# Kernel optimization log

Measured on AMD Instinct MI355X. Metric: run time of the kernel, lower is better.

Reference implementation:

```python
import jax, jax.numpy as jnp
import numpy as np

# static config (matches init_kwargs and spatial_shapes input)
SPATIAL = ((100, 100), (50, 50), (25, 25), (13, 13))  # (H, W) per level
D_MODEL, N_HEADS, N_LEVELS, N_POINTS, D_FFN = 256, 8, 4, 4, 1024
D_HEAD = D_MODEL // N_HEADS
LEN_IN = sum(h * w for h, w in SPATIAL)
LEVEL_START = np.cumsum([0] + [h * w for h, w in SPATIAL])[:-1]


def setup_inputs() -> dict:
    key = jax.random.key(0)
    ks = jax.random.split(key, 12)
    N = 2
    f = lambda k, shape, s=0.02: jax.random.normal(k, shape, jnp.float32) * s
    return {
        "src": jax.random.normal(ks[0], (N, LEN_IN, D_MODEL), jnp.float32),
        "pos": jax.random.normal(ks[1], (N, LEN_IN, D_MODEL), jnp.float32),
        "reference_points": jax.random.uniform(ks[2], (N, LEN_IN, N_LEVELS, 2), jnp.float32),
        "spatial_shapes": jnp.asarray(SPATIAL, jnp.int32),
        "level_start_index": jnp.asarray(LEVEL_START, jnp.int32),
        "W_value": f(ks[3], (D_MODEL, D_MODEL)),
        "b_value": jnp.zeros((D_MODEL,), jnp.float32),
        "W_off": f(ks[4], (D_MODEL, N_HEADS * N_LEVELS * N_POINTS * 2)),
        "b_off": f(ks[5], (N_HEADS * N_LEVELS * N_POINTS * 2,), 0.5),
        "W_attn": f(ks[6], (D_MODEL, N_HEADS * N_LEVELS * N_POINTS)),
        "b_attn": jnp.zeros((N_HEADS * N_LEVELS * N_POINTS,), jnp.float32),
        "W_out": f(ks[7], (D_MODEL, D_MODEL)),
        "b_out": jnp.zeros((D_MODEL,), jnp.float32),
        "W1": f(ks[8], (D_MODEL, D_FFN)),
        "b1": jnp.zeros((D_FFN,), jnp.float32),
        "W2": f(ks[9], (D_FFN, D_MODEL)),
        "b2": jnp.zeros((D_MODEL,), jnp.float32),
        "g1": jnp.ones((D_MODEL,), jnp.float32),
        "be1": jnp.zeros((D_MODEL,), jnp.float32),
        "g2": jnp.ones((D_MODEL,), jnp.float32),
        "be2": jnp.zeros((D_MODEL,), jnp.float32),
    }


def _ln(x, g, b, eps=1e-5):
    mu = x.mean(-1, keepdims=True)
    var = ((x - mu) ** 2).mean(-1, keepdims=True)
    return (x - mu) * jax.lax.rsqrt(var + eps) * g + b


def _bilinear(v, loc, H, W):
    # v: [N, heads, H*W, Dh]; loc: [N, Lq, heads, P, 2] normalized to [0,1]
    # replicates F.grid_sample(align_corners=False, padding_mode='zeros') with grid=2*loc-1
    N, Lq, Hh, P, _ = loc.shape
    x = loc[..., 0] * W - 0.5
    y = loc[..., 1] * H - 0.5
    x0 = jnp.floor(x)
    y0 = jnp.floor(y)
    wx1 = x - x0
    wy1 = y - y0
    x0i = x0.astype(jnp.int32)
    y0i = y0.astype(jnp.int32)
    out = jnp.zeros((N, Lq, Hh, P, v.shape[-1]), v.dtype)
    for dy, dx in ((0, 0), (0, 1), (1, 0), (1, 1)):
        xi = x0i + dx
        yi = y0i + dy
        w = (wx1 if dx else 1.0 - wx1) * (wy1 if dy else 1.0 - wy1)
        valid = (xi >= 0) & (xi < W) & (yi >= 0) & (yi < H)
        idx = jnp.clip(yi, 0, H - 1) * W + jnp.clip(xi, 0, W - 1)  # [N,Lq,Hh,P]
        idx = idx.transpose(0, 2, 1, 3).reshape(N, Hh, Lq * P)
        g = jax.vmap(jax.vmap(lambda vm, im: vm[im]))(v, idx)  # [N,Hh,Lq*P,Dh]
        g = g.reshape(N, Hh, Lq, P, -1).transpose(0, 2, 1, 3, 4)
        out = out + (w * valid)[..., None] * g
    return out


def reference(src, pos, reference_points, spatial_shapes, level_start_index,
              W_value, b_value, W_off, b_off, W_attn, b_attn, W_out, b_out,
              W1, b1, W2, b2, g1, be1, g2, be2):
    N, Lq, _ = src.shape
    value = (src @ W_value + b_value).reshape(N, Lq, N_HEADS, D_HEAD)
    q = src + pos  # with_pos_embed
    off = (q @ W_off + b_off).reshape(N, Lq, N_HEADS, N_LEVELS, N_POINTS, 2)
    attn = (q @ W_attn + b_attn).reshape(N, Lq, N_HEADS, N_LEVELS * N_POINTS)
    attn = jax.nn.softmax(attn, axis=-1).reshape(N, Lq, N_HEADS, N_LEVELS, N_POINTS)
    # offset_normalizer = (W, H) per level
    normalizer = jnp.asarray([[w, h] for h, w in SPATIAL], jnp.float32)
    loc = reference_points[:, :, None, :, None, :] + off / normalizer[None, None, None, :, None, :]
    out = jnp.zeros((N, Lq, N_HEADS, D_HEAD), jnp.float32)
    for l, (H, W) in enumerate(SPATIAL):
        s = int(LEVEL_START[l])
        v_l = value[:, s:s + H * W].transpose(0, 2, 1, 3)  # [N, heads, H*W, Dh]
        samp = _bilinear(v_l, loc[:, :, :, l], H, W)       # [N, Lq, heads, P, Dh]
        out = out + jnp.einsum('nqhp,nqhpc->nqhc', attn[:, :, :, l], samp)
    src2 = out.reshape(N, Lq, D_MODEL) @ W_out + b_out
    x = _ln(src + src2, g1, be1)
    ffn = jax.nn.relu(x @ W1 + b1) @ W2 + b2
    return _ln(x + ffn, g2, be2)
```

## Files before the change

kernel.cpp:

```cpp
#include <hip/hip_runtime.h>
#include <hip/hip_bf16.h>
#include <cstdint>

#define D_MODEL   256
#define N_HEADS   8
#define N_LEVELS  4
#define N_POINTS  4
#define D_FFN     1024
#define D_HEAD    32
#define LEN_IN    13294
#define NBATCH    2
#define M_TOK     (NBATCH * LEN_IN)
#define M_PAD     26624

__constant__ int c_lvl_h[4] = {100, 50, 25, 13};
__constant__ int c_lvl_w[4] = {100, 50, 25, 13};
__constant__ int c_lvl_s[4] = {0, 10000, 12500, 13125};

typedef __attribute__((ext_vector_type(8))) __bf16 bf16x8;
typedef __attribute__((ext_vector_type(4))) __bf16 bf16x4;
typedef __attribute__((ext_vector_type(2))) __bf16 bf16x2;
typedef __attribute__((ext_vector_type(4))) float  f32x4;
typedef __attribute__((ext_vector_type(4))) uint32_t u32x4;

__device__ __forceinline__ float bflo(uint32_t w) { return __uint_as_float(w << 16); }
__device__ __forceinline__ float bfhi(uint32_t w) { return __uint_as_float(w & 0xffff0000u); }

__device__ __forceinline__ void lds_direct16(const void* g, void* l) {
    __builtin_amdgcn_global_load_lds(
        (const __attribute__((address_space(1))) uint32_t*)(uintptr_t)g,
        (__attribute__((address_space(3))) uint32_t*)(uintptr_t)l,
        16, 0, 0);
}

__global__ __launch_bounds__(256) void cvt_src_q(
    const float4* __restrict__ src, const float4* __restrict__ pos,
    bf16x4* __restrict__ sb, bf16x4* __restrict__ qb, int n4)
{
    const int i = blockIdx.x * 256 + threadIdx.x;
    if (i >= n4) return;
    const float4 s = src[i];
    const float4 p = pos[i];
    bf16x4 sv = { (__bf16)s.x, (__bf16)s.y, (__bf16)s.z, (__bf16)s.w };
    bf16x4 qv = { (__bf16)(s.x + p.x), (__bf16)(s.y + p.y),
                  (__bf16)(s.z + p.z), (__bf16)(s.w + p.w) };
    sb[i] = sv;
    qb[i] = qv;
}

__global__ __launch_bounds__(256) void transpose_all(
    const float* __restrict__ s0, const float* __restrict__ s1, const float* __restrict__ s2,
    const float* __restrict__ s3, const float* __restrict__ s4, const float* __restrict__ s5,
    __bf16* __restrict__ d0, __bf16* __restrict__ d1, __bf16* __restrict__ d2,
    __bf16* __restrict__ d3, __bf16* __restrict__ d4, __bf16* __restrict__ d5,
    const float* __restrict__ b_off, const float* __restrict__ b_attn,
    float* __restrict__ bias_oa)
{
    const int tx = threadIdx.x;
    const int ty = threadIdx.y;
    const int tid = ty * 32 + tx;
    const int b = blockIdx.x;
    if (b == 736) {
        if (tid < 256) bias_oa[tid] = b_off[tid];
        if (tid < 128) bias_oa[256 + tid] = b_attn[tid];
        return;
    }
    const int starts[7] = {0, 64, 128, 160, 224, 480, 736};
    const int Ks[6] = {256, 256, 256, 256, 256, 1024};
    const int Ns[6] = {256, 256, 128, 256, 1024, 256};
    const float* srcs[6] = {s0, s1, s2, s3, s4, s5};
    __bf16* dsts[6] = {d0, d1, d2, d3, d4, d5};
    int i = 0;
    while (b >= starts[i + 1]) ++i;
    const int t = b - starts[i];
    const int K = Ks[i], N = Ns[i];
    const float* W = srcs[i];
    __bf16* Wt = dsts[i];
    const int ntx = N >> 5;
    const int n0 = (t % ntx) * 32;
    const int k0 = (t / ntx) * 32;

    __shared__ float tl[32][33];
    #pragma unroll
    for (int j = 0; j < 4; ++j)
        tl[ty + j * 8][tx] = W[(size_t)(k0 + ty + j * 8) * N + n0 + tx];
    __syncthreads();
    #pragma unroll
    for (int j = 0; j < 4; ++j)
        Wt[(size_t)(n0 + ty + j * 8) * K + k0 + tx] = (__bf16)tl[tx][ty + j * 8];
}

template <typename OutT, bool RELU, int NP, int K>
__global__ __launch_bounds__(256) void gemm_mfma(
    const __bf16* __restrict__ A, const __bf16* __restrict__ Bt,
    const float* __restrict__ bias, OutT* __restrict__ C,
    int M, int N)
{
    __shared__ __bf16 As[NP * 128 * 32];
    __shared__ __bf16 Bs[NP * 128 * 32];

    const int tid  = threadIdx.x;
    const int lane = tid & 63;
    const int wv   = tid >> 6;
    const int bm   = blockIdx.y * 128;
    const int bn   = blockIdx.x * 128;
    const int wm   = (wv >> 1) * 64;
    const int wn   = (wv & 1) * 64;
    const int srow = lane >> 2;
    const int skc  = (lane & 3) * 8;
    const int fm   = lane & 15;
    const int fko  = (lane >> 4) * 8;

    f32x4 acc[4][4] = {};

    #pragma unroll
    for (int k0 = 0; k0 < K; k0 += 32 * NP) {
        #pragma unroll
        for (int p = 0; p < NP; ++p) {
            #pragma unroll
            for (int c = 0; c < 2; ++c) {
                const int r = wv * 32 + c * 16;
                lds_direct16(A  + (size_t)(bm + r + srow) * K + k0 + p * 32 + skc, As + p * 4096 + r * 32);
                lds_direct16(Bt + (size_t)(bn + r + srow) * K + k0 + p * 32 + skc, Bs + p * 4096 + r * 32);
            }
        }
        __syncthreads();

        #pragma unroll
        for (int p = 0; p < NP; ++p) {
            bf16x8 af[4], bfr[4];
            #pragma unroll
            for (int t = 0; t < 4; ++t) {
                af[t]  = *(const bf16x8*)(As + p * 4096 + (wm + t * 16 + fm) * 32 + fko);
                bfr[t] = *(const bf16x8*)(Bs + p * 4096 + (wn + t * 16 + fm) * 32 + fko);
            }
            #pragma unroll
            for (int mt = 0; mt < 4; ++mt)
                #pragma unroll
                for (int nt = 0; nt < 4; ++nt)
                    acc[mt][nt] = __builtin_amdgcn_mfma_f32_16x16x32_bf16(
                        af[mt], bfr[nt], acc[mt][nt], 0, 0, 0);
        }
        __syncthreads();
    }

    const int ecol = lane & 15;
    const int erow = (lane >> 4) * 4;
    #pragma unroll
    for (int nt = 0; nt < 4; ++nt) {
        const int col = bn + wn + nt * 16 + ecol;
        const float bv = bias[col];
        #pragma unroll
        for (int mt = 0; mt < 4; ++mt) {
            #pragma unroll
            for (int r = 0; r < 4; ++r) {
                const int row = bm + wm + mt * 16 + erow + r;
                if (row < M) {
                    float v = acc[mt][nt][r] + bv;
                    if (RELU) v = fmaxf(v, 0.f);
                    C[(size_t)row * N + col] = (OutT)v;
                }
            }
        }
    }
}

struct alignas(8) IW { uint32_t idx; float wt; };

__global__ __launch_bounds__(256) void msda_sample(
    const __bf16* __restrict__ value,
    const __bf16* __restrict__ oa,
    const float* __restrict__ refp,
    __bf16* __restrict__ out)
{
    __shared__ IW    sc[8][16][4];
    __shared__ float sw[8][16];

    const int row = blockIdx.x;
    const int tid = threadIdx.x;

    uint32_t cidx[4];
    float    cwt[4];
    const int h  = tid >> 4;
    const int lp = tid & 15;

    if (tid < 128) {
        const int l  = lp >> 2;
        const int Ww = c_lvl_w[l];
        const int Hh = c_lvl_h[l];
        const uint32_t opk = *(const uint32_t*)(oa + (size_t)row * 384 + h * 32 + lp * 2);
        const float ox = bflo(opk), oy = bfhi(opk);
        const float rx = refp[((size_t)row * 4 + l) * 2 + 0];
        const float ry = refp[((size_t)row * 4 + l) * 2 + 1];
        const float x = (rx + ox / (float)Ww) * (float)Ww - 0.5f;
        const float y = (ry + oy / (float)Hh) * (float)Hh - 0.5f;
        const float xf = floorf(x), yf = floorf(y);
        const float fx = x - xf,    fy = y - yf;
        const int x0 = (int)xf, y0 = (int)yf;
        const int n  = row / LEN_IN;
        const int base = n * LEN_IN + c_lvl_s[l];
        #pragma unroll
        for (int c = 0; c < 4; ++c) {
            const int dx = c & 1, dy = c >> 1;
            const int xi = x0 + dx, yi = y0 + dy;
            const bool valid = (xi >= 0) & (xi < Ww) & (yi >= 0) & (yi < Hh);
            cidx[c] = valid ? (uint32_t)(base + yi * Ww + xi) * 256u : 0u;
            cwt[c]  = valid ? (dx ? fx : 1.f - fx) * (dy ? fy : 1.f - fy) : 0.f;
        }
    } else if (tid < 136) {
        const int h2 = tid - 128;
        const __bf16* ap = oa + (size_t)row * 384 + 256 + h2 * 16;
        float e[16], mx = -1e30f;
        #pragma unroll
        for (int i = 0; i < 16; ++i) { e[i] = (float)ap[i]; mx = fmaxf(mx, e[i]); }
        float s = 0.f;
        #pragma unroll
        for (int i = 0; i < 16; ++i) { e[i] = __expf(e[i] - mx); s += e[i]; }
        const float inv = 1.f / s;
        #pragma unroll
        for (int i = 0; i < 16; ++i) sw[h2][i] = e[i] * inv;
    }
    __syncthreads();
    if (tid < 128) {
        const float a = sw[h][lp];
        IW w0 = { cidx[0], cwt[0] * a };
        IW w1 = { cidx[1], cwt[1] * a };
        IW w2 = { cidx[2], cwt[2] * a };
        IW w3 = { cidx[3], cwt[3] * a };
        u32x4 pk0 = { w0.idx, __float_as_uint(w0.wt), w1.idx, __float_as_uint(w1.wt) };
        u32x4 pk1 = { w2.idx, __float_as_uint(w2.wt), w3.idx, __float_as_uint(w3.wt) };
        *(u32x4*)&sc[h][lp][0] = pk0;
        *(u32x4*)&sc[h][lp][2] = pk1;
    }
    __syncthreads();

    const uint16_t* __restrict__ vu = (const uint16_t*)value;
    const int gh  = tid >> 5;
    const uint32_t col = (uint32_t)tid;
    float acc = 0.f;
    #pragma unroll
    for (int q = 0; q < 16; ++q) {
        const u32x4 a = *(const u32x4*)&sc[gh][q][0];
        const u32x4 b = *(const u32x4*)&sc[gh][q][2];
        acc += __uint_as_float(a.y) * __uint_as_float((uint32_t)vu[a.x + col] << 16);
        acc += __uint_as_float(a.w) * __uint_as_float((uint32_t)vu[a.z + col] << 16);
        acc += __uint_as_float(b.y) * __uint_as_float((uint32_t)vu[b.x + col] << 16);
        acc += __uint_as_float(b.w) * __uint_as_float((uint32_t)vu[b.z + col] << 16);
    }
    out[(size_t)row * 256 + tid] = (__bf16)acc;
}

template <bool BF16OUT, bool BBF16>
__global__ __launch_bounds__(256) void add_ln(
    const float4* __restrict__ a, const void* __restrict__ braw,
    const float4* __restrict__ g4, const float4* __restrict__ be4,
    float4* __restrict__ out, bf16x4* __restrict__ outb)
{
    const int tid  = threadIdx.x;
    const int row  = blockIdx.x * 4 + (tid >> 6);
    const int lane = tid & 63;
    const size_t e = (size_t)row * 64 + lane;
    const float4 va = a[e];
    float4 vb;
    if (BBF16) {
        const bf16x4 t = ((const bf16x4*)braw)[e];
        vb = { (float)t[0], (float)t[1], (float)t[2], (float)t[3] };
    } else {
        vb = ((const float4*)braw)[e];
    }
    float4 v = { va.x + vb.x, va.y + vb.y, va.z + vb.z, va.w + vb.w };

    float s  = v.x + v.y + v.z + v.w;
    float s2 = v.x * v.x + v.y * v.y + v.z * v.z + v.w * v.w;
    #pragma unroll
    for (int o = 32; o > 0; o >>= 1) {
        s  += __shfl_down(s, o);
        s2 += __shfl_down(s2, o);
    }
    s  = __shfl(s, 0);
    s2 = __shfl(s2, 0);
    const float mu  = s * (1.f / 256.f);
    const float var = s2 * (1.f / 256.f) - mu * mu;
    const float rs  = rsqrtf(var + 1e-5f);
    const float4 g = g4[lane];
    const float4 be = be4[lane];
    float4 o;
    o.x = (v.x - mu) * rs * g.x + be.x;
    o.y = (v.y - mu) * rs * g.y + be.y;
    o.z = (v.z - mu) * rs * g.z + be.z;
    o.w = (v.w - mu) * rs * g.w + be.w;
    out[e] = o;
    if (BF16OUT) {
        bf16x4 ob = { (__bf16)o.x, (__bf16)o.y, (__bf16)o.z, (__bf16)o.w };
        outb[e] = ob;
    }
}

extern "C" void kernel_launch(void* const* d_in, const int* in_sizes, int n_in,
                              void* d_out, int out_size, void* d_ws, size_t ws_size,
                              hipStream_t stream)
{
    const float* src     = (const float*)d_in[0];
    const float* pos     = (const float*)d_in[1];
    const float* refp    = (const float*)d_in[2];
    const float* W_value = (const float*)d_in[5];
    const float* b_value = (const float*)d_in[6];
    const float* W_off   = (const float*)d_in[7];
    const float* b_off   = (const float*)d_in[8];
    const float* W_attn  = (const float*)d_in[9];
    const float* b_attn  = (const float*)d_in[10];
    const float* W_out   = (const float*)d_in[11];
    const float* b_out   = (const float*)d_in[12];
    const float* W1      = (const float*)d_in[13];
    const float* b1      = (const float*)d_in[14];
    const float* W2      = (const float*)d_in[15];
    const float* b2      = (const float*)d_in[16];
    const float* g1      = (const float*)d_in[17];
    const float* be1     = (const float*)d_in[18];
    const float* g2      = (const float*)d_in[19];
    const float* be2     = (const float*)d_in[20];
    float* outp = (float*)d_out;

    const int M = M_TOK;
    char* ws = (char*)d_ws;
    const size_t R2 = (size_t)M_PAD * 512;

    __bf16* src_b = (__bf16*)(ws);
    __bf16* q_b   = (__bf16*)(ws + R2);
    __bf16* val_b = (__bf16*)(ws + 2 * R2);
    __bf16* oa    = (__bf16*)(ws + 3 * R2);
    __bf16* samp  = (__bf16*)(ws + 9 * R2 / 2);
    __bf16* src2b = (__bf16*)(ws + 11 * R2 / 2);
    __bf16* f2b   = (__bf16*)(ws + 11 * R2 / 2);
    float*  x     = (float*)(ws + 13 * R2 / 2);
    __bf16* x_b   = (__bf16*)(ws + 17 * R2 / 2);
    __bf16* hbuf  = (__bf16*)(ws);
    __bf16* wbase = (__bf16*)(ws + 19 * R2 / 2);
    __bf16* Wt_value = wbase;
    __bf16* Wt_oa    = wbase + 65536;
    __bf16* Wt_out   = wbase + 163840;
    __bf16* Wt1      = wbase + 229376;
    __bf16* Wt2      = wbase + 491520;
    float*  bias_oa  = (float*)(wbase + 753664);

    const dim3 blk(256);
    const int n4 = M * 256 / 4;

    cvt_src_q<<<dim3((n4 + 255) / 256), blk, 0, stream>>>(
        (const float4*)src, (const float4*)pos, (bf16x4*)src_b, (bf16x4*)q_b, n4);
    transpose_all<<<dim3(737), dim3(32, 8), 0, stream>>>(
        W_value, W_off, W_attn, W_out, W1, W2,
        Wt_value, Wt_oa, Wt_oa + 65536, Wt_out, Wt1, Wt2,
        b_off, b_attn, bias_oa);

    const int gm = M_PAD / 128;

    gemm_mfma<__bf16, false, 2, 256><<<dim3(2, gm), blk, 0, stream>>>(src_b, Wt_value, b_value, val_b, M, 256);
    gemm_mfma<__bf16, false, 2, 256><<<dim3(3, gm), blk, 0, stream>>>(q_b,   Wt_oa,    bias_oa, oa,    M, 384);

    msda_sample<<<dim3(M), blk, 0, stream>>>(val_b, oa, refp, samp);

    gemm_mfma<__bf16, false, 2, 256><<<dim3(2, gm), blk, 0, stream>>>(samp, Wt_out, b_out, src2b, M, 256);
    add_ln<true, true><<<dim3(M / 4), blk, 0, stream>>>(
        (const float4*)src, (const void*)src2b, (const float4*)g1, (const float4*)be1,
        (float4*)x, (bf16x4*)x_b);
    gemm_mfma<__bf16, true,  2, 256><<<dim3(8, gm), blk, 0, stream>>>(x_b,  Wt1, b1, hbuf, M, 1024);
    gemm_mfma<__bf16, false, 2, 1024><<<dim3(2, gm), blk, 0, stream>>>(hbuf, Wt2, b2, f2b, M, 256);
    add_ln<false, true><<<dim3(M / 4), blk, 0, stream>>>(
        (const float4*)x, (const void*)f2b, (const float4*)g2, (const float4*)be2,
        (float4*)outp, nullptr);
}
```

Baseline: 349.5 us.

## Fuse layernorms into output GEMMs and merge prep and front GEMM launches

Merges the weight-transpose and src/pos conversion kernels into one launch, and runs the value and offset/attention projections as one GEMM grid. Adds a gemm_ln kernel that computes a full 256-column row tile, then adds bias and residual and applies LayerNorm in the epilogue. This replaces the separate add_ln passes and drops the fp32 intermediate x buffer. The residuals are now read from bf16 copies (src_b, x_b) instead of fp32, which costs some accuracy. The sampler switches to byte-offset indexing and unrolling is dropped on the GEMM K loop.

```diff
diff --git a/kernel.cpp b/kernel.cpp
--- a/kernel.cpp
+++ b/kernel.cpp
@@ -19,7 +19,6 @@
 
 typedef __attribute__((ext_vector_type(8))) __bf16 bf16x8;
 typedef __attribute__((ext_vector_type(4))) __bf16 bf16x4;
-typedef __attribute__((ext_vector_type(2))) __bf16 bf16x2;
 typedef __attribute__((ext_vector_type(4))) float  f32x4;
 typedef __attribute__((ext_vector_type(4))) uint32_t u32x4;
 
@@ -33,38 +32,37 @@
         16, 0, 0);
 }
 
-__global__ __launch_bounds__(256) void cvt_src_q(
-    const float4* __restrict__ src, const float4* __restrict__ pos,
-    bf16x4* __restrict__ sb, bf16x4* __restrict__ qb, int n4)
-{
-    const int i = blockIdx.x * 256 + threadIdx.x;
-    if (i >= n4) return;
-    const float4 s = src[i];
-    const float4 p = pos[i];
-    bf16x4 sv = { (__bf16)s.x, (__bf16)s.y, (__bf16)s.z, (__bf16)s.w };
-    bf16x4 qv = { (__bf16)(s.x + p.x), (__bf16)(s.y + p.y),
-                  (__bf16)(s.z + p.z), (__bf16)(s.w + p.w) };
-    sb[i] = sv;
-    qb[i] = qv;
-}
-
-__global__ __launch_bounds__(256) void transpose_all(
+__global__ __launch_bounds__(256) void prep(
     const float* __restrict__ s0, const float* __restrict__ s1, const float* __restrict__ s2,
     const float* __restrict__ s3, const float* __restrict__ s4, const float* __restrict__ s5,
     __bf16* __restrict__ d0, __bf16* __restrict__ d1, __bf16* __restrict__ d2,
     __bf16* __restrict__ d3, __bf16* __restrict__ d4, __bf16* __restrict__ d5,
     const float* __restrict__ b_off, const float* __restrict__ b_attn,
-    float* __restrict__ bias_oa)
-{
-    const int tx = threadIdx.x;
-    const int ty = threadIdx.y;
-    const int tid = ty * 32 + tx;
+    float* __restrict__ bias_oa,
+    const float4* __restrict__ src, const float4* __restrict__ pos,
+    bf16x4* __restrict__ sb, bf16x4* __restrict__ qb, int n4)
+{
+    const int tid = threadIdx.x;
     const int b = blockIdx.x;
+    if (b >= 737) {
+        const int i = (b - 737) * 256 + tid;
+        if (i >= n4) return;
+        const float4 s = src[i];
+        const float4 p = pos[i];
+        bf16x4 sv = { (__bf16)s.x, (__bf16)s.y, (__bf16)s.z, (__bf16)s.w };
+        bf16x4 qv = { (__bf16)(s.x + p.x), (__bf16)(s.y + p.y),
+                      (__bf16)(s.z + p.z), (__bf16)(s.w + p.w) };
+        sb[i] = sv;
+        qb[i] = qv;
+        return;
+    }
     if (b == 736) {
         if (tid < 256) bias_oa[tid] = b_off[tid];
         if (tid < 128) bias_oa[256 + tid] = b_attn[tid];
         return;
     }
+    const int tx = tid & 31;
+    const int ty = tid >> 5;
     const int starts[7] = {0, 64, 128, 160, 224, 480, 736};
     const int Ks[6] = {256, 256, 256, 256, 256, 1024};
     const int Ns[6] = {256, 256, 128, 256, 1024, 256};
@@ -91,10 +89,10 @@
 }
 
 template <typename OutT, bool RELU, int NP, int K>
-__global__ __launch_bounds__(256) void gemm_mfma(
+__device__ __forceinline__ void gemm_core(
     const __bf16* __restrict__ A, const __bf16* __restrict__ Bt,
     const float* __restrict__ bias, OutT* __restrict__ C,
-    int M, int N)
+    int M, int N, int bm, int bn)
 {
     __shared__ __bf16 As[NP * 128 * 32];
     __shared__ __bf16 Bs[NP * 128 * 32];
@@ -102,8 +100,6 @@
     const int tid  = threadIdx.x;
     const int lane = tid & 63;
     const int wv   = tid >> 6;
-    const int bm   = blockIdx.y * 128;
-    const int bn   = blockIdx.x * 128;
     const int wm   = (wv >> 1) * 64;
     const int wn   = (wv & 1) * 64;
     const int srow = lane >> 2;
@@ -113,7 +109,6 @@
 
     f32x4 acc[4][4] = {};
 
-    #pragma unroll
     for (int k0 = 0; k0 < K; k0 += 32 * NP) {
         #pragma unroll
         for (int p = 0; p < NP; ++p) {
@@ -165,7 +160,155 @@
     }
 }
 
-struct alignas(8) IW { uint32_t idx; float wt; };
+template <typename OutT, bool RELU, int NP, int K>
+__global__ __launch_bounds__(256) void gemm_mfma(
+    const __bf16* __restrict__ A, const __bf16* __restrict__ Bt,
+    const float* __restrict__ bias, OutT* __restrict__ C, int M, int N)
+{
+    gemm_core<OutT, RELU, NP, K>(A, Bt, bias, C, M, N, blockIdx.y * 128, blockIdx.x * 128);
+}
+
+__global__ __launch_bounds__(256) void gemm_front(
+    const __bf16* __restrict__ A0, const __bf16* __restrict__ B0,
+    const float* __restrict__ bi0, __bf16* __restrict__ C0,
+    const __bf16* __restrict__ A1, const __bf16* __restrict__ B1,
+    const float* __restrict__ bi1, __bf16* __restrict__ C1, int M)
+{
+    const int bx = blockIdx.x;
+    if (bx < 2)
+        gemm_core<__bf16, false, 2, 256>(A0, B0, bi0, C0, M, 256, blockIdx.y * 128, bx * 128);
+    else
+        gemm_core<__bf16, false, 2, 256>(A1, B1, bi1, C1, M, 384, blockIdx.y * 128, (bx - 2) * 128);
+}
+
+template <typename OutT, int K>
+__global__ __launch_bounds__(256) void gemm_ln(
+    const __bf16* __restrict__ A, const __bf16* __restrict__ Bt,
+    const float* __restrict__ bias, const __bf16* __restrict__ res,
+    const float* __restrict__ gamma, const float* __restrict__ beta,
+    OutT* __restrict__ Cout, int M)
+{
+    constexpr int NP = 2;
+    __shared__ __bf16 As[NP * 64 * 32];
+    __shared__ __bf16 Bs[NP * 256 * 32];
+    __shared__ float lnsum[64][4];
+    __shared__ float lnsq[64][4];
+    __shared__ float lnstat[64][2];
+
+    const int tid  = threadIdx.x;
+    const int lane = tid & 63;
+    const int wv   = tid >> 6;
+    const int bm   = blockIdx.x * 64;
+    const int wn   = wv * 64;
+    const int srow = lane >> 2;
+    const int skc  = (lane & 3) * 8;
+    const int fm   = lane & 15;
+    const int fko  = (lane >> 4) * 8;
+
+    f32x4 acc[4][4] = {};
+
+    for (int k0 = 0; k0 < K; k0 += 32 * NP) {
+        #pragma unroll
+        for (int p = 0; p < NP; ++p) {
+            if (wv == 0) {  }
+            lds_direct16(A + (size_t)(bm + wv * 16 + srow) * K + k0 + p * 32 + skc,
+                         As + p * 2048 + (wv * 16) * 32);
+            #pragma unroll
+            for (int c = 0; c < 4; ++c) {
+                const int r = wv * 64 + c * 16;
+                lds_direct16(Bt + (size_t)(r + srow) * K + k0 + p * 32 + skc,
+                             Bs + p * 8192 + r * 32);
+            }
+        }
+        __syncthreads();
+
+        #pragma unroll
+        for (int p = 0; p < NP; ++p) {
+            bf16x8 af[4], bfr[4];
+            #pragma unroll
+            for (int t = 0; t < 4; ++t) {
+                af[t]  = *(const bf16x8*)(As + p * 2048 + (t * 16 + fm) * 32 + fko);
+                bfr[t] = *(const bf16x8*)(Bs + p * 8192 + (wn + t * 16 + fm) * 32 + fko);
+            }
+            #pragma unroll
+            for (int mt = 0; mt < 4; ++mt)
+                #pragma unroll
+                for (int nt = 0; nt < 4; ++nt)
+                    acc[mt][nt] = __builtin_amdgcn_mfma_f32_16x16x32_bf16(
+                        af[mt], bfr[nt], acc[mt][nt], 0, 0, 0);
+        }
+        __syncthreads();
+    }
+
+    const int ecol = lane & 15;
+    const int erow = (lane >> 4) * 4;
+
+    float g4[4], b4[4];
+    #pragma unroll
+    for (int nt = 0; nt < 4; ++nt) {
+        const int col = wn + nt * 16 + ecol;
+        g4[nt] = gamma[col];
+        b4[nt] = beta[col];
+        const float bv = bias[col];
+        #pragma unroll
+        for (int mt = 0; mt < 4; ++mt) {
+            #pragma unroll
+            for (int r = 0; r < 4; ++r) {
+                const int row = bm + mt * 16 + erow + r;
+                acc[mt][nt][r] += bv + (float)res[(size_t)row * 256 + col];
+            }
+        }
+    }
+
+    #pragma unroll
+    for (int mt = 0; mt < 4; ++mt) {
+        #pragma unroll
+        for (int r = 0; r < 4; ++r) {
+            float s  = acc[mt][0][r] + acc[mt][1][r] + acc[mt][2][r] + acc[mt][3][r];
+            float s2 = acc[mt][0][r] * acc[mt][0][r] + acc[mt][1][r] * acc[mt][1][r]
+                     + acc[mt][2][r] * acc[mt][2][r] + acc[mt][3][r] * acc[mt][3][r];
+            #pragma unroll
+            for (int o = 1; o < 16; o <<= 1) {
+                s  += __shfl_xor(s, o);
+                s2 += __shfl_xor(s2, o);
+            }
+            if (ecol == 0) {
+                const int rl = mt * 16 + erow + r;
+                lnsum[rl][wv] = s;
+                lnsq[rl][wv]  = s2;
+            }
+        }
+    }
+    __syncthreads();
+    if (tid < 64) {
+        const float s  = lnsum[tid][0] + lnsum[tid][1] + lnsum[tid][2] + lnsum[tid][3];
+        const float s2 = lnsq[tid][0] + lnsq[tid][1] + lnsq[tid][2] + lnsq[tid][3];
+        const float mu = s * (1.f / 256.f);
+        const float var = s2 * (1.f / 256.f) - mu * mu;
+        lnstat[tid][0] = mu;
+        lnstat[tid][1] = rsqrtf(var + 1e-5f);
+    }
+    __syncthreads();
+
+    #pragma unroll
+    for (int mt = 0; mt < 4; ++mt) {
+        #pragma unroll
+        for (int r = 0; r < 4; ++r) {
+            const int rl = mt * 16 + erow + r;
+            const int row = bm + rl;
+            const float mu = lnstat[rl][0];
+            const float rs = lnstat[rl][1];
+            if (row < M) {
+                #pragma unroll
+                for (int nt = 0; nt < 4; ++nt) {
+                    const int col = wn + nt * 16 + ecol;
+                    const float o = (acc[mt][nt][r] - mu) * rs * g4[nt] + b4[nt];
+                    Cout[(size_t)row * 256 + col] = (OutT)o;
+                }
+            }
+        }
+    }
+}
 
 __global__ __launch_bounds__(256) void msda_sample(
     const __bf16* __restrict__ value,
@@ -173,7 +316,7 @@
     const float* __restrict__ refp,
     __bf16* __restrict__ out)
 {
-    __shared__ IW    sc[8][16][4];
+    __shared__ uint32_t sc[8][16][8];
     __shared__ float sw[8][16];
 
     const int row = blockIdx.x;
@@ -204,7 +347,7 @@
             const int dx = c & 1, dy = c >> 1;
             const int xi = x0 + dx, yi = y0 + dy;
             const bool valid = (xi >= 0) & (xi < Ww) & (yi >= 0) & (yi < Hh);
-            cidx[c] = valid ? (uint32_t)(base + yi * Ww + xi) * 256u : 0u;
+            cidx[c] = valid ? (uint32_t)(base + yi * Ww + xi) * 512u : 0u;
             cwt[c]  = valid ? (dx ? fx : 1.f - fx) * (dy ? fy : 1.f - fy) : 0.f;
         }
     } else if (tid < 136) {
@@ -223,77 +366,27 @@
     __syncthreads();
     if (tid < 128) {
         const float a = sw[h][lp];
-        IW w0 = { cidx[0], cwt[0] * a };
-        IW w1 = { cidx[1], cwt[1] * a };
-        IW w2 = { cidx[2], cwt[2] * a };
-        IW w3 = { cidx[3], cwt[3] * a };
-        u32x4 pk0 = { w0.idx, __float_as_uint(w0.wt), w1.idx, __float_as_uint(w1.wt) };
-        u32x4 pk1 = { w2.idx, __float_as_uint(w2.wt), w3.idx, __float_as_uint(w3.wt) };
+        u32x4 pk0 = { cidx[0], __float_as_uint(cwt[0] * a), cidx[1], __float_as_uint(cwt[1] * a) };
+        u32x4 pk1 = { cidx[2], __float_as_uint(cwt[2] * a), cidx[3], __float_as_uint(cwt[3] * a) };
         *(u32x4*)&sc[h][lp][0] = pk0;
-        *(u32x4*)&sc[h][lp][2] = pk1;
+        *(u32x4*)&sc[h][lp][4] = pk1;
     }
     __syncthreads();
 
-    const uint16_t* __restrict__ vu = (const uint16_t*)value;
+    const char* __restrict__ vb = (const char*)value;
     const int gh  = tid >> 5;
-    const uint32_t col = (uint32_t)tid;
+    const uint32_t colb = (uint32_t)tid * 2u;
     float acc = 0.f;
     #pragma unroll
     for (int q = 0; q < 16; ++q) {
         const u32x4 a = *(const u32x4*)&sc[gh][q][0];
-        const u32x4 b = *(const u32x4*)&sc[gh][q][2];
-        acc += __uint_as_float(a.y) * __uint_as_float((uint32_t)vu[a.x + col] << 16);
-        acc += __uint_as_float(a.w) * __uint_as_float((uint32_t)vu[a.z + col] << 16);
-        acc += __uint_as_float(b.y) * __uint_as_float((uint32_t)vu[b.x + col] << 16);
-        acc += __uint_as_float(b.w) * __uint_as_float((uint32_t)vu[b.z + col] << 16);
+        const u32x4 b = *(const u32x4*)&sc[gh][q][4];
+        acc += __uint_as_float(a.y) * __uint_as_float((uint32_t)(*(const uint16_t*)(vb + (size_t)(a.x + colb))) << 16);
+        acc += __uint_as_float(a.w) * __uint_as_float((uint32_t)(*(const uint16_t*)(vb + (size_t)(a.z + colb))) << 16);
+        acc += __uint_as_float(b.y) * __uint_as_float((uint32_t)(*(const uint16_t*)(vb + (size_t)(b.x + colb))) << 16);
+        acc += __uint_as_float(b.w) * __uint_as_float((uint32_t)(*(const uint16_t*)(vb + (size_t)(b.z + colb))) << 16);
     }
     out[(size_t)row * 256 + tid] = (__bf16)acc;
-}
-
-template <bool BF16OUT, bool BBF16>
-__global__ __launch_bounds__(256) void add_ln(
-    const float4* __restrict__ a, const void* __restrict__ braw,
-    const float4* __restrict__ g4, const float4* __restrict__ be4,
-    float4* __restrict__ out, bf16x4* __restrict__ outb)
-{
-    const int tid  = threadIdx.x;
-    const int row  = blockIdx.x * 4 + (tid >> 6);
-    const int lane = tid & 63;
-    const size_t e = (size_t)row * 64 + lane;
-    const float4 va = a[e];
-    float4 vb;
-    if (BBF16) {
-        const bf16x4 t = ((const bf16x4*)braw)[e];
-        vb = { (float)t[0], (float)t[1], (float)t[2], (float)t[3] };
-    } else {
-        vb = ((const float4*)braw)[e];
-    }
-    float4 v = { va.x + vb.x, va.y + vb.y, va.z + vb.z, va.w + vb.w };
-
-    float s  = v.x + v.y + v.z + v.w;
-    float s2 = v.x * v.x + v.y * v.y + v.z * v.z + v.w * v.w;
-    #pragma unroll
-    for (int o = 32; o > 0; o >>= 1) {
-        s  += __shfl_down(s, o);
-        s2 += __shfl_down(s2, o);
-    }
-    s  = __shfl(s, 0);
-    s2 = __shfl(s2, 0);
-    const float mu  = s * (1.f / 256.f);
-    const float var = s2 * (1.f / 256.f) - mu * mu;
-    const float rs  = rsqrtf(var + 1e-5f);
-    const float4 g = g4[lane];
-    const float4 be = be4[lane];
-    float4 o;
-    o.x = (v.x - mu) * rs * g.x + be.x;
-    o.y = (v.y - mu) * rs * g.y + be.y;
-    o.z = (v.z - mu) * rs * g.z + be.z;
-    o.w = (v.w - mu) * rs * g.w + be.w;
-    out[e] = o;
-    if (BF16OUT) {
-        bf16x4 ob = { (__bf16)o.x, (__bf16)o.y, (__bf16)o.z, (__bf16)o.w };
-        outb[e] = ob;
-    }
 }
 
 extern "C" void kernel_launch(void* const* d_in, const int* in_sizes, int n_in,
@@ -330,12 +423,9 @@
     __bf16* val_b = (__bf16*)(ws + 2 * R2);
     __bf16* oa    = (__bf16*)(ws + 3 * R2);
     __bf16* samp  = (__bf16*)(ws + 9 * R2 / 2);
-    __bf16* src2b = (__bf16*)(ws + 11 * R2 / 2);
-    __bf16* f2b   = (__bf16*)(ws + 11 * R2 / 2);
-    float*  x     = (float*)(ws + 13 * R2 / 2);
-    __bf16* x_b   = (__bf16*)(ws + 17 * R2 / 2);
+    __bf16* x_b   = (__bf16*)(ws + 11 * R2 / 2);
     __bf16* hbuf  = (__bf16*)(ws);
-    __bf16* wbase = (__bf16*)(ws + 19 * R2 / 2);
+    __bf16* wbase = (__bf16*)(ws + 13 * R2 / 2);
     __bf16* Wt_value = wbase;
     __bf16* Wt_oa    = wbase + 65536;
     __bf16* Wt_out   = wbase + 163840;
@@ -345,28 +435,26 @@
 
     const dim3 blk(256);
     const int n4 = M * 256 / 4;
-
-    cvt_src_q<<<dim3((n4 + 255) / 256), blk, 0, stream>>>(
-        (const float4*)src, (const float4*)pos, (bf16x4*)src_b, (bf16x4*)q_b, n4);
-    transpose_all<<<dim3(737), dim3(32, 8), 0, stream>>>(
+    const int gm = M_PAD / 128;
+    const int gl = M_PAD / 64;
+
+    prep<<<dim3(737 + (n4 + 255) / 256), blk, 0, stream>>>(
         W_value, W_off, W_attn, W_out, W1, W2,
         Wt_value, Wt_oa, Wt_oa + 65536, Wt_out, Wt1, Wt2,
-        b_off, b_attn, bias_oa);
-
-    const int gm = M_PAD / 128;
-
-    gemm_mfma<__bf16, false, 2, 256><<<dim3(2, gm), blk, 0, stream>>>(src_b, Wt_value, b_value, val_b, M, 256);
-    gemm_mfma<__bf16, false, 2, 256><<<dim3(3, gm), blk, 0, stream>>>(q_b,   Wt_oa,    bias_oa, oa,    M, 384);
+        b_off, b_attn, bias_oa,
+        (const float4*)src, (const float4*)pos, (bf16x4*)src_b, (bf16x4*)q_b, n4);
+
+    gemm_front<<<dim3(5, gm), blk, 0, stream>>>(
+        src_b, Wt_value, b_value, val_b,
+        q_b,   Wt_oa,    bias_oa, oa, M);
 
     msda_sample<<<dim3(M), blk, 0, stream>>>(val_b, oa, refp, samp);
 
-    gemm_mfma<__bf16, false, 2, 256><<<dim3(2, gm), blk, 0, stream>>>(samp, Wt_out, b_out, src2b, M, 256);
-    add_ln<true, true><<<dim3(M / 4), blk, 0, stream>>>(
-        (const float4*)src, (const void*)src2b, (const float4*)g1, (const float4*)be1,
-        (float4*)x, (bf16x4*)x_b);
-    gemm_mfma<__bf16, true,  2, 256><<<dim3(8, gm), blk, 0, stream>>>(x_b,  Wt1, b1, hbuf, M, 1024);
-    gemm_mfma<__bf16, false, 2, 1024><<<dim3(2, gm), blk, 0, stream>>>(hbuf, Wt2, b2, f2b, M, 256);
-    add_ln<false, true><<<dim3(M / 4), blk, 0, stream>>>(
-        (const float4*)x, (const void*)f2b, (const float4*)g2, (const float4*)be2,
-        (float4*)outp, nullptr);
-}
+    gemm_ln<__bf16, 256><<<dim3(gl), blk, 0, stream>>>(
+        samp, Wt_out, b_out, src_b, g1, be1, x_b, M);
+
+    gemm_mfma<__bf16, true, 2, 256><<<dim3(8, gm), blk, 0, stream>>>(x_b, Wt1, b1, hbuf, M, 1024);
+
+    gemm_ln<float, 1024><<<dim3(gl), blk, 0, stream>>>(
+        hbuf, Wt2, b2, x_b, g2, be2, outp, M);
+}
```

Result: no change. 348.2 us (-0.4%).
